# Kernel tuning notes

Measured on AMD Instinct MI355X. Metric: run time of the kernel, lower is better.

Reference implementation:

```python
import jax, jax.numpy as jnp
import numpy as np

S = 64            # rendered_size
CLASS_NUM = 14    # dataset.enc_len
NEG_SLOPE = 0.01
EPS = 1e-5


def _conv(x, w, stride, pad):
    return jax.lax.conv_general_dilated(
        x, w, (stride, stride), [(pad, pad), (pad, pad)],
        dimension_numbers=("NCHW", "OIHW", "NCHW"))


def _bn(x, gamma, beta):
    # BatchNorm2d in training mode: biased batch stats over (N,H,W)
    m = jnp.mean(x, axis=(0, 2, 3), keepdims=True)
    v = jnp.var(x, axis=(0, 2, 3), keepdims=True)
    xn = (x - m) * jax.lax.rsqrt(v + EPS)
    return xn * gamma.reshape(1, -1, 1, 1) + beta.reshape(1, -1, 1, 1)


def _lrelu(x):
    return jnp.where(x >= 0, x, NEG_SLOPE * x)


def _render(elements):
    # elements: (B, N, class_num+4)
    rects = elements[:, :, -4:]
    cls = elements[:, :, :-4]                       # (B, N, C)
    x = rects[:, :, 0][:, :, None, None] * S        # (B, N, 1, 1)
    y = rects[:, :, 1][:, :, None, None] * S
    w = rects[:, :, 2][:, :, None, None] * S
    h = rects[:, :, 3][:, :, None, None] * S
    x0, x1 = x - 0.5 * w, x + 0.5 * w
    y0, y1 = y - 0.5 * h, y + 0.5 * h
    cx = jnp.arange(S, dtype=elements.dtype)[None, None, None, :]  # varies along W
    cy = jnp.arange(S, dtype=elements.dtype)[None, None, :, None]  # varies along H
    k = lambda c, cr: jnp.maximum(1.0 - jnp.abs(c - cr), 0.0)
    b0 = lambda c, cr: jnp.clip(c - cr, 0.0, 1.0)
    b1 = lambda cr, c: jnp.clip(cr - c, 0.0, 1.0)
    by = b0(cy, y0) * b1(y1, cy)                    # (B, N, S, S)
    bx = b0(cx, x0) * b1(x1, cx)
    l0 = k(cx, x0) * by
    l1 = k(cx, x1) * by
    l2 = k(cy, y0) * bx
    l3 = k(cy, y1) * bx
    rendered = jnp.maximum(jnp.maximum(l0, l1), jnp.maximum(l2, l3))  # (B,N,S,S)
    # sum over elements of class one-hot * rendered -> (B, C, S, S)
    return jnp.einsum("bnc,bnhw->bchw", cls, rendered)


def setup_inputs() -> dict:
    key = jax.random.key(0)
    ks = jax.random.split(key, 8)
    B, N = 64, 46
    inp = {
        "input_data": jax.random.uniform(ks[0], (B, N, CLASS_NUM + 4), dtype=jnp.float32),
        "input_length": jax.random.randint(ks[1], (B,), 0, N, dtype=jnp.int32),
        # cnn convs (bias=False) + BN affine params
        "w1": jax.random.normal(ks[2], (64, CLASS_NUM, 5, 5), jnp.float32) * 0.05,
        "g1": jnp.ones((64,), jnp.float32), "b1": jnp.zeros((64,), jnp.float32),
        "w2": jax.random.normal(ks[3], (128, 64, 5, 5), jnp.float32) * 0.03,
        "g2": jnp.ones((128,), jnp.float32), "b2": jnp.zeros((128,), jnp.float32),
        "w3": jax.random.normal(ks[4], (256, 128, 5, 5), jnp.float32) * 0.02,
        "g3": jnp.ones((256,), jnp.float32), "b3": jnp.zeros((256,), jnp.float32),
        # classifier: conv k=8 (bias=False) + BN + 1x1 conv (bias=True)
        "w4": jax.random.normal(ks[5], (1024, 256, 8, 8), jnp.float32) * 0.01,
        "g4": jnp.ones((1024,), jnp.float32), "b4": jnp.zeros((1024,), jnp.float32),
        "w5": jax.random.normal(ks[6], (1, 1024, 1, 1), jnp.float32) * 0.03,
        "b5": jnp.zeros((1,), jnp.float32),
    }
    return inp


def reference(input_data, input_length, w1, g1, b1, w2, g2, b2,
              w3, g3, b3, w4, g4, b4, w5, b5):
    rendered = _render(input_data)                       # (B, C, 64, 64)
    h = _lrelu(_bn(_conv(rendered, w1, 2, 2), g1, b1))   # (B, 64, 32, 32)
    h = _lrelu(_bn(_conv(h, w2, 2, 2), g2, b2))          # (B, 128, 16, 16)
    h = _lrelu(_bn(_conv(h, w3, 2, 2), g3, b3))          # (B, 256, 8, 8)
    h = _lrelu(_bn(_conv(h, w4, 1, 0), g4, b4))          # (B, 1024, 1, 1)
    out = _conv(h, w5, 1, 0) + b5.reshape(1, -1, 1, 1)   # (B, 1, 1, 1)
    return out.squeeze()                                 # (B,)
```

## Files before the change

### kernel.cpp

```cpp
#include <hip/hip_runtime.h>
#include <hip/hip_bf16.h>

#define NEG 0.01f
#define EPS 1e-5f

typedef __attribute__((ext_vector_type(8))) short short8;
typedef __attribute__((ext_vector_type(4))) float floatx4;

__device__ inline unsigned short f2bf(float f) {
    __hip_bfloat16 h = __float2bfloat16(f);
    union { __hip_bfloat16 h; unsigned short u; } cv; cv.h = h;
    return cv.u;
}

__global__ __launch_bounds__(256) void render_kernel(const float* __restrict__ in,
                                                     unsigned short* __restrict__ out) {
    int b = blockIdx.x >> 4;
    int chunk = blockIdx.x & 15;
    __shared__ float r0[46], r1[46], r2[46], r3[46];
    __shared__ float cls_s[46 * 14];
    int tid = threadIdx.x;
    if (tid < 46) {
        const float* p = in + ((size_t)b * 46 + tid) * 18 + 14;
        float x = p[0] * 64.f, y = p[1] * 64.f, w = p[2] * 64.f, h = p[3] * 64.f;
        r0[tid] = x - 0.5f * w; r1[tid] = x + 0.5f * w;
        r2[tid] = y - 0.5f * h; r3[tid] = y + 0.5f * h;
    }
    for (int idx = tid; idx < 46 * 14; idx += 256) {
        int n = idx / 14, c = idx % 14;
        cls_s[idx] = in[((size_t)b * 46 + n) * 18 + c];
    }
    __syncthreads();
    if (tid < 33) {
        int j = chunk * 33 + tid;
        if (j < 528) {
            int y, x;
            if (j < 136) { y = j / 68; x = j - y * 68; }
            else if (j < 272) { int t = j - 136; int yy = t / 68; y = 66 + yy; x = t - yy * 68; }
            else { int t = j - 272; y = 2 + (t >> 2); int k = t & 3; x = (k < 2) ? k : 64 + k; }
            size_t zb = (((size_t)b * 68 + y) * 68 + x) * 16;
            short8 z;
#pragma unroll
            for (int i = 0; i < 8; ++i) z[i] = 0;
            *(short8*)(out + zb) = z;
            *(short8*)(out + zb + 8) = z;
        }
    }
    int pix = chunk * 256 + tid;
    float cx = (float)(pix & 63);
    float cy = (float)(pix >> 6);
    float acc[14];
#pragma unroll
    for (int c = 0; c < 14; ++c) acc[c] = 0.f;
    for (int n = 0; n < 46; ++n) {
        float x0 = r0[n], x1 = r1[n], y0 = r2[n], y1 = r3[n];
        float by = fminf(fmaxf(cy - y0, 0.f), 1.f) * fminf(fmaxf(y1 - cy, 0.f), 1.f);
        float bx = fminf(fmaxf(cx - x0, 0.f), 1.f) * fminf(fmaxf(x1 - cx, 0.f), 1.f);
        float kx0 = fmaxf(1.f - fabsf(cx - x0), 0.f);
        float kx1 = fmaxf(1.f - fabsf(cx - x1), 0.f);
        float ky0 = fmaxf(1.f - fabsf(cy - y0), 0.f);
        float ky1 = fmaxf(1.f - fabsf(cy - y1), 0.f);
        float r = fmaxf(fmaxf(kx0 * by, kx1 * by), fmaxf(ky0 * bx, ky1 * bx));
        if (r > 0.f) {
#pragma unroll
            for (int c = 0; c < 14; ++c) acc[c] = fmaf(cls_s[n * 14 + c], r, acc[c]);
        }
    }
    size_t obase = (((size_t)b * 68 + ((pix >> 6) + 2)) * 68 + ((pix & 63) + 2)) * 16;
    short8 v0, v1;
#pragma unroll
    for (int i = 0; i < 8; ++i) v0[i] = (short)f2bf(acc[i]);
#pragma unroll
    for (int i = 0; i < 6; ++i) v1[i] = (short)f2bf(acc[8 + i]);
    v1[6] = 0; v1[7] = 0;
    *(short8*)(out + obase) = v0;
    *(short8*)(out + obase + 8) = v1;
}

__global__ __launch_bounds__(256) void wtrans_all(const float* __restrict__ w1,
                                                  const float* __restrict__ w2,
                                                  const float* __restrict__ w3,
                                                  unsigned short* __restrict__ wT1,
                                                  unsigned short* __restrict__ wT2,
                                                  unsigned short* __restrict__ wT3) {
    int idx = blockIdx.x * 256 + threadIdx.x;
    const float* w; unsigned short* wT; int CIN, CPLOG, SUB, COLOG;
    if (idx < 30720) { w = w1; wT = wT1; CIN = 14; CPLOG = 4; SUB = 3; COLOG = 6; }
    else if (idx < 235520) { idx -= 30720; w = w2; wT = wT2; CIN = 64; CPLOG = 6; SUB = 10; COLOG = 7; }
    else if (idx < 1054720) { idx -= 235520; w = w3; wT = wT3; CIN = 128; CPLOG = 7; SUB = 20; COLOG = 8; }
    else return;
    int kk = idx & 31;
    int co = (idx >> 5) & ((1 << COLOG) - 1);
    int s = idx >> (5 + COLOG);
    int kh = s / SUB, sub = s - kh * SUB;
    int kidx = sub * 32 + kk;
    int kw = kidx >> CPLOG;
    int ci = kidx & ((1 << CPLOG) - 1);
    float v = (kw < 5 && ci < CIN) ? w[((size_t)(co * CIN + ci) * 5 + kh) * 5 + kw] : 0.f;
    wT[idx] = f2bf(v);
}

template <int CP, int COUT, int HP, int LOG_OHW, int LOG_OW, int SUB,
          int NCO, int NT, int CH, int NW>
__global__ __launch_bounds__(NW * 64) void conv_mfma(
        const unsigned short* __restrict__ inP,
        const unsigned short* __restrict__ wT,
        float* __restrict__ outX,
        float* __restrict__ stacc) {
    constexpr int NSTEP = 5 * SUB;
    constexpr int NCHUNK = NSTEP / CH;
    constexpr int COT = NT * 16;
    constexpr int NSTG = (CH * COT * 4) / (NW * 64);
    static_assert(NSTEP % CH == 0, "CH must divide NSTEP");
    static_assert((CH * COT * 4) % (NW * 64) == 0, "staging must tile evenly");
    __shared__ short Bs[2][CH][COT][32];
    __shared__ float sred[NW][2][COT];
    int tid = threadIdx.x;
    int wave = tid >> 6, lane = tid & 63, q = lane >> 4, l16 = lane & 15;
    int bm = blockIdx.x / NCO, bco = blockIdx.x % NCO;

    const short* aB[4];
#pragma unroll
    for (int f = 0; f < 4; ++f) {
        int m = bm * (NW * 64) + wave * 64 + f * 16 + l16;
        int b = m >> LOG_OHW;
        int ohw = m & ((1 << LOG_OHW) - 1);
        int oh = ohw >> LOG_OW, ow = ohw & ((1 << LOG_OW) - 1);
        aB[f] = (const short*)inP + ((size_t)((b * HP + 2 * oh) * HP + 2 * ow)) * CP + q * 8;
    }
    const short* bgbase = (const short*)wT + (size_t)bco * COT * 32;

    floatx4 acc[4][NT];
#pragma unroll
    for (int f = 0; f < 4; ++f)
#pragma unroll
        for (int nt = 0; nt < NT; ++nt) acc[f][nt] = (floatx4){0.f, 0.f, 0.f, 0.f};

    short8 nb[NSTG];
#pragma unroll
    for (int i = 0; i < NSTG; ++i) {
        int v = tid + i * NW * 64;
        int s = v / (COT * 4);
        int rem = v - s * (COT * 4);
        nb[i] = *(const short8*)(bgbase + ((size_t)s * COUT) * 32 + rem * 8);
    }
#pragma unroll
    for (int i = 0; i < NSTG; ++i) {
        int v = tid + i * NW * 64;
        int s = v / (COT * 4);
        int rem = v - s * (COT * 4);
        *(short8*)((short*)&Bs[0][s][0][0] + rem * 8) = nb[i];
    }
    __syncthreads();

    for (int chunk = 0; chunk < NCHUNK; ++chunk) {
        int cur = chunk & 1;
        if (chunk + 1 < NCHUNK) {
            int step0 = (chunk + 1) * CH;
#pragma unroll
            for (int i = 0; i < NSTG; ++i) {
                int v = tid + i * NW * 64;
                int s = v / (COT * 4);
                int rem = v - s * (COT * 4);
                nb[i] = *(const short8*)(bgbase + ((size_t)(step0 + s) * COUT) * 32 + rem * 8);
            }
        }
#pragma unroll
        for (int s = 0; s < CH; ++s) {
            int step = chunk * CH + s;
            int kh = step / SUB, sub = step - kh * SUB;
            short8 af[4];
#pragma unroll
            for (int f = 0; f < 4; ++f)
                af[f] = *(const short8*)(aB[f] + (size_t)(kh * HP) * CP + sub * 32);
#pragma unroll
            for (int nt = 0; nt < NT; ++nt) {
                short8 bf = *(const short8*)&Bs[cur][s][nt * 16 + l16][q * 8];
#pragma unroll
                for (int f = 0; f < 4; ++f)
                    acc[f][nt] = __builtin_amdgcn_mfma_f32_16x16x32_bf16(af[f], bf, acc[f][nt], 0, 0, 0);
            }
        }
        if (chunk + 1 < NCHUNK) {
#pragma unroll
            for (int i = 0; i < NSTG; ++i) {
                int v = tid + i * NW * 64;
                int s = v / (COT * 4);
                int rem = v - s * (COT * 4);
                *(short8*)((short*)&Bs[cur ^ 1][s][0][0] + rem * 8) = nb[i];
            }
            __syncthreads();
        }
    }
#pragma unroll
    for (int f = 0; f < 4; ++f)
#pragma unroll
        for (int nt = 0; nt < NT; ++nt)
#pragma unroll
            for (int rg = 0; rg < 4; ++rg) {
                int mg = bm * (NW * 64) + wave * 64 + f * 16 + q * 4 + rg;
                int co = bco * COT + nt * 16 + l16;
                outX[(size_t)mg * COUT + co] = acc[f][nt][rg];
            }
#pragma unroll
    for (int nt = 0; nt < NT; ++nt) {
        float s = 0.f, s2 = 0.f;
#pragma unroll
        for (int f = 0; f < 4; ++f)
#pragma unroll
            for (int rg = 0; rg < 4; ++rg) {
                float v = acc[f][nt][rg];
                s += v; s2 = fmaf(v, v, s2);
            }
        s += __shfl_xor(s, 16); s += __shfl_xor(s, 32);
        s2 += __shfl_xor(s2, 16); s2 += __shfl_xor(s2, 32);
        if (q == 0) {
            sred[wave][0][nt * 16 + l16] = s;
            sred[wave][1][nt * 16 + l16] = s2;
        }
    }
    __syncthreads();
    if (tid < COT) {
        float ts = 0.f, ts2 = 0.f;
#pragma unroll
        for (int w = 0; w < NW; ++w) { ts += sred[w][0][tid]; ts2 += sred[w][1][tid]; }
        atomicAdd(&stacc[bco * COT + tid], ts);
        atomicAdd(&stacc[COUT + bco * COT + tid], ts2);
    }
}

__global__ __launch_bounds__(256) void conv4_mfma(const unsigned short* __restrict__ A,
                                                  const float* __restrict__ w4,
                                                  float* __restrict__ h4) {
    constexpr int CH = 4, NCHUNK = 8;
    __shared__ short Bs[CH][64][40];
    int tid = threadIdx.x;
    int bco = blockIdx.x & 15;
    int ks = blockIdx.x >> 4;
    int wave = tid >> 6, lane = tid & 63, q = lane >> 4, l16 = lane & 15;
    const short* aBase = (const short*)A + (size_t)(wave * 16 + l16) * 16384 + ks * 1024 + q * 8;
    int r = tid >> 2, cc = tid & 3;
    const float* bg = w4 + (size_t)(bco * 64 + r) * 16384 + ks * 1024 + cc * 8;

    floatx4 acc[4];
#pragma unroll
    for (int nt = 0; nt < 4; ++nt) acc[nt] = (floatx4){0.f, 0.f, 0.f, 0.f};

    short8 nb[CH];
#pragma unroll
    for (int s = 0; s < CH; ++s) {
        float4 b0 = *(const float4*)(bg + s * 32);
        float4 b1 = *(const float4*)(bg + s * 32 + 4);
        nb[s][0] = (short)f2bf(b0.x); nb[s][1] = (short)f2bf(b0.y);
        nb[s][2] = (short)f2bf(b0.z); nb[s][3] = (short)f2bf(b0.w);
        nb[s][4] = (short)f2bf(b1.x); nb[s][5] = (short)f2bf(b1.y);
        nb[s][6] = (short)f2bf(b1.z); nb[s][7] = (short)f2bf(b1.w);
    }
#pragma unroll
    for (int s = 0; s < CH; ++s) *(short8*)&Bs[s][r][cc * 8] = nb[s];
    __syncthreads();

    for (int chunk = 0; chunk < NCHUNK; ++chunk) {
        bool has_next = (chunk + 1 < NCHUNK);
        if (has_next) {
#pragma unroll
            for (int s = 0; s < CH; ++s) {
                int step = (chunk + 1) * CH + s;
                float4 b0 = *(const float4*)(bg + step * 32);
                float4 b1 = *(const float4*)(bg + step * 32 + 4);
                nb[s][0] = (short)f2bf(b0.x); nb[s][1] = (short)f2bf(b0.y);
                nb[s][2] = (short)f2bf(b0.z); nb[s][3] = (short)f2bf(b0.w);
                nb[s][4] = (short)f2bf(b1.x); nb[s][5] = (short)f2bf(b1.y);
                nb[s][6] = (short)f2bf(b1.z); nb[s][7] = (short)f2bf(b1.w);
            }
        }
#pragma unroll
        for (int s = 0; s < CH; ++s) {
            int step = chunk * CH + s;
            short8 af = *(const short8*)(aBase + step * 32);
#pragma unroll
            for (int nt = 0; nt < 4; ++nt) {
                short8 bf = *(const short8*)&Bs[s][nt * 16 + l16][q * 8];
                acc[nt] = __builtin_amdgcn_mfma_f32_16x16x32_bf16(af, bf, acc[nt], 0, 0, 0);
            }
        }
        if (has_next) {
            __syncthreads();
#pragma unroll
            for (int s = 0; s < CH; ++s) *(short8*)&Bs[s][r][cc * 8] = nb[s];
            __syncthreads();
        }
    }
#pragma unroll
    for (int nt = 0; nt < 4; ++nt) {
#pragma unroll
        for (int rg = 0; rg < 4; ++rg) {
            int mg = wave * 16 + q * 4 + rg;
            int co = bco * 64 + nt * 16 + l16;
            atomicAdd(&h4[(size_t)mg * 1024 + co], acc[nt][rg]);
        }
    }
}

__global__ __launch_bounds__(256) void stats_part(const float* __restrict__ X,
                                                  float* __restrict__ acc,
                                                  int CO, int R, int RPB, int CGLOG) {
    int tid = threadIdx.x;
    int cg = blockIdx.x & ((1 << CGLOG) - 1);
    int rb = blockIdx.x >> CGLOG;
    int c = (cg << 6) + (tid & 63);
    int w = tid >> 6;
    float s = 0.f, s2 = 0.f;
    int rend = min(R, (rb + 1) * RPB);
    for (int r = rb * RPB + w; r < rend; r += 4) {
        float v = X[(size_t)r * CO + c];
        s += v; s2 += v * v;
    }
    __shared__ float ls[4][64], ls2[4][64];
    ls[w][tid & 63] = s; ls2[w][tid & 63] = s2;
    __syncthreads();
    if (tid < 64) {
        float ts = ls[0][tid] + ls[1][tid] + ls[2][tid] + ls[3][tid];
        float ts2 = ls2[0][tid] + ls2[1][tid] + ls2[2][tid] + ls2[3][tid];
        int cc = (cg << 6) + tid;
        atomicAdd(&acc[cc], ts);
        atomicAdd(&acc[CO + cc], ts2);
    }
}

__global__ __launch_bounds__(256) void bnpad_kernel(const float* __restrict__ X,
                                                    const float* __restrict__ stacc,
                                                    const float* __restrict__ g,
                                                    const float* __restrict__ bb,
                                                    unsigned short* __restrict__ out,
                                                    int CO_LOG, int OH, int OHP,
                                                    float invN, int total) {
    int idx = blockIdx.x * 256 + threadIdx.x;
    if (idx >= total) return;
    int CO = 1 << CO_LOG;
    int c = idx & (CO - 1);
    float mean = stacc[c] * invN;
    float var = fmaxf(stacc[CO + c] * invN - mean * mean, 0.f);
    float sc = g[c] * rsqrtf(var + EPS);
    float sh = bb[c] - mean * sc;
    int t = idx >> CO_LOG;
    int x = t % OHP; t /= OHP;
    int y = t % OHP; int b = t / OHP;
    unsigned short v = 0;
    if (y >= 2 && y < OH + 2 && x >= 2 && x < OH + 2) {
        float f = X[(((size_t)(b * OH + (y - 2)) * OH + (x - 2)) << CO_LOG) + c];
        f = f * sc + sh;
        f = f >= 0.f ? f : NEG * f;
        v = f2bf(f);
    }
    out[idx] = v;
}

__global__ __launch_bounds__(256) void bn_nchw_kernel(const float* __restrict__ X,
                                                      const float* __restrict__ stacc,
                                                      const float* __restrict__ g,
                                                      const float* __restrict__ bb,
                                                      unsigned short* __restrict__ out,
                                                      int total) {
    int idx = blockIdx.x * 256 + threadIdx.x;
    if (idx >= total) return;
    int hw = idx & 63;
    int ci = (idx >> 6) & 255;
    int b = idx >> 14;
    float mean = stacc[ci] * (1.f / 4096.f);
    float var = fmaxf(stacc[256 + ci] * (1.f / 4096.f) - mean * mean, 0.f);
    float sc = g[ci] * rsqrtf(var + EPS);
    float sh = bb[ci] - mean * sc;
    float f = X[((size_t)(b * 64 + hw)) * 256 + ci] * sc + sh;
    f = f >= 0.f ? f : NEG * f;
    out[idx] = f2bf(f);
}

__global__ __launch_bounds__(256) void conv5_kernel(const float* __restrict__ X,
                                                    const float* __restrict__ stacc,
                                                    const float* __restrict__ g,
                                                    const float* __restrict__ bb,
                                                    const float* __restrict__ w5,
                                                    const float* __restrict__ b5,
                                                    float* __restrict__ out) {
    int b = blockIdx.x, tid = threadIdx.x;
    float s = 0.f;
    for (int c = tid; c < 1024; c += 256) {
        float mean = stacc[c] * (1.f / 64.f);
        float var = fmaxf(stacc[1024 + c] * (1.f / 64.f) - mean * mean, 0.f);
        float sc = g[c] * rsqrtf(var + EPS);
        float sh = bb[c] - mean * sc;
        float f = X[(size_t)b * 1024 + c] * sc + sh;
        f = f >= 0.f ? f : NEG * f;
        s = fmaf(f, w5[c], s);
    }
#pragma unroll
    for (int off = 32; off > 0; off >>= 1) s += __shfl_down(s, off);
    __shared__ float ls[4];
    if ((tid & 63) == 0) ls[tid >> 6] = s;
    __syncthreads();
    if (tid == 0) out[b] = ls[0] + ls[1] + ls[2] + ls[3] + b5[0];
}

extern "C" void kernel_launch(void* const* d_in, const int* in_sizes, int n_in,
                              void* d_out, int out_size, void* d_ws, size_t ws_size,
                              hipStream_t stream) {
    (void)in_sizes; (void)n_in; (void)out_size; (void)ws_size;
    const float* input_data = (const float*)d_in[0];
    const float* w1 = (const float*)d_in[2];
    const float* g1 = (const float*)d_in[3];
    const float* b1 = (const float*)d_in[4];
    const float* w2 = (const float*)d_in[5];
    const float* g2 = (const float*)d_in[6];
    const float* b2 = (const float*)d_in[7];
    const float* w3 = (const float*)d_in[8];
    const float* g3 = (const float*)d_in[9];
    const float* b3 = (const float*)d_in[10];
    const float* w4 = (const float*)d_in[11];
    const float* g4 = (const float*)d_in[12];
    const float* b4 = (const float*)d_in[13];
    const float* w5 = (const float*)d_in[14];
    const float* b5 = (const float*)d_in[15];

    char* ws = (char*)d_ws;
    float* regA = (float*)ws;
    char* wsB = ws + 16777216;
    char* wsC = wsB + 10616832;
    char* wsD = wsC + 9469952;
    float* h4  = (float*)wsD;
    float* st1 = (float*)(wsD + 262144);
    float* st2 = (float*)(wsD + 262656);
    float* st3 = (float*)(wsD + 263680);
    float* st4 = (float*)(wsD + 265728);
    unsigned short* wT1 = (unsigned short*)(wsD + 274432);
    unsigned short* wT2 = (unsigned short*)(wsD + 335872);
    unsigned short* wT3 = (unsigned short*)(wsD + 745472);

    unsigned short* rendered = (unsigned short*)wsC;
    float* conv1out = regA;
    unsigned short* pad1 = (unsigned short*)wsB;
    float* conv2out = (float*)wsC;
    unsigned short* pad2 = (unsigned short*)wsB;
    float* conv3out = regA;
    unsigned short* a4 = (unsigned short*)wsC;

    hipMemsetAsync(wsD, 0, 273920, stream);
    wtrans_all<<<4120, 256, 0, stream>>>(w1, w2, w3, wT1, wT2, wT3);
    render_kernel<<<1024, 256, 0, stream>>>(input_data, rendered);

    conv_mfma<16, 64, 68, 10, 5, 3, 1, 4, 5, 4><<<256, 256, 0, stream>>>(rendered, wT1, conv1out, st1);
    bnpad_kernel<<<20736, 256, 0, stream>>>(conv1out, st1, g1, b1, pad1, 6, 32, 36, 1.f / 65536.f, 5308416);

    conv_mfma<64, 128, 36, 8, 4, 10, 4, 2, 10, 4><<<256, 256, 0, stream>>>(pad1, wT2, conv2out, st2);
    bnpad_kernel<<<12800, 256, 0, stream>>>(conv2out, st2, g2, b2, pad2, 7, 16, 20, 1.f / 16384.f, 3276800);

    conv_mfma<128, 256, 20, 6, 3, 20, 8, 2, 10, 2><<<256, 128, 0, stream>>>(pad2, wT3, conv3out, st3);
    bn_nchw_kernel<<<4096, 256, 0, stream>>>(conv3out, st3, g3, b3, a4, 1048576);

    conv4_mfma<<<256, 256, 0, stream>>>(a4, w4, h4);
    stats_part<<<16, 256, 0, stream>>>(h4, st4, 1024, 64, 64, 4);

    conv5_kernel<<<64, 256, 0, stream>>>(h4, st4, g4, b4, w5, b5, (float*)d_out);
}
```

Measured before the change: 280.5 us.

## Merge setup kernels, pad LDS weight tiles, halve conv block sizes, fold BN4 stats

Merges the weight-transpose and render kernels into one launch. Pads the shared-memory B tile rows from 32 to 40 shorts to avoid bank conflicts. Retunes the three conv launches to use half the waves per block, twice the blocks and smaller chunks, and doubles the conv4 chunk size. Removes the separate stats kernel by having every conv5 block recompute the per-channel BN statistics itself, which trades a launch for redundant reads of h4.

```diff
diff --git a/kernel.cpp b/kernel.cpp
--- a/kernel.cpp
+++ b/kernel.cpp
@@ -13,12 +13,36 @@
     return cv.u;
 }
 
-__global__ __launch_bounds__(256) void render_kernel(const float* __restrict__ in,
-                                                     unsigned short* __restrict__ out) {
+__global__ __launch_bounds__(256) void head_kernel(const float* __restrict__ in,
+                                                   unsigned short* __restrict__ out,
+                                                   const float* __restrict__ w1,
+                                                   const float* __restrict__ w2,
+                                                   const float* __restrict__ w3,
+                                                   unsigned short* __restrict__ wT1,
+                                                   unsigned short* __restrict__ wT2,
+                                                   unsigned short* __restrict__ wT3) {
+    __shared__ float r0[46], r1[46], r2[46], r3[46];
+    __shared__ float cls_s[46 * 14];
+    if (blockIdx.x >= 1024) {
+        int idx = (blockIdx.x - 1024) * 256 + threadIdx.x;
+        const float* w; unsigned short* wT; int CIN, CPLOG, SUB, COLOG;
+        if (idx < 30720) { w = w1; wT = wT1; CIN = 14; CPLOG = 4; SUB = 3; COLOG = 6; }
+        else if (idx < 235520) { idx -= 30720; w = w2; wT = wT2; CIN = 64; CPLOG = 6; SUB = 10; COLOG = 7; }
+        else if (idx < 1054720) { idx -= 235520; w = w3; wT = wT3; CIN = 128; CPLOG = 7; SUB = 20; COLOG = 8; }
+        else return;
+        int kk = idx & 31;
+        int co = (idx >> 5) & ((1 << COLOG) - 1);
+        int s = idx >> (5 + COLOG);
+        int kh = s / SUB, sub = s - kh * SUB;
+        int kidx = sub * 32 + kk;
+        int kw = kidx >> CPLOG;
+        int ci = kidx & ((1 << CPLOG) - 1);
+        float v = (kw < 5 && ci < CIN) ? w[((size_t)(co * CIN + ci) * 5 + kh) * 5 + kw] : 0.f;
+        wT[idx] = f2bf(v);
+        return;
+    }
     int b = blockIdx.x >> 4;
     int chunk = blockIdx.x & 15;
-    __shared__ float r0[46], r1[46], r2[46], r3[46];
-    __shared__ float cls_s[46 * 14];
     int tid = threadIdx.x;
     if (tid < 46) {
         const float* p = in + ((size_t)b * 46 + tid) * 18 + 14;
@@ -75,29 +99,6 @@
     v1[6] = 0; v1[7] = 0;
     *(short8*)(out + obase) = v0;
     *(short8*)(out + obase + 8) = v1;
-}
-
-__global__ __launch_bounds__(256) void wtrans_all(const float* __restrict__ w1,
-                                                  const float* __restrict__ w2,
-                                                  const float* __restrict__ w3,
-                                                  unsigned short* __restrict__ wT1,
-                                                  unsigned short* __restrict__ wT2,
-                                                  unsigned short* __restrict__ wT3) {
-    int idx = blockIdx.x * 256 + threadIdx.x;
-    const float* w; unsigned short* wT; int CIN, CPLOG, SUB, COLOG;
-    if (idx < 30720) { w = w1; wT = wT1; CIN = 14; CPLOG = 4; SUB = 3; COLOG = 6; }
-    else if (idx < 235520) { idx -= 30720; w = w2; wT = wT2; CIN = 64; CPLOG = 6; SUB = 10; COLOG = 7; }
-    else if (idx < 1054720) { idx -= 235520; w = w3; wT = wT3; CIN = 128; CPLOG = 7; SUB = 20; COLOG = 8; }
-    else return;
-    int kk = idx & 31;
-    int co = (idx >> 5) & ((1 << COLOG) - 1);
-    int s = idx >> (5 + COLOG);
-    int kh = s / SUB, sub = s - kh * SUB;
-    int kidx = sub * 32 + kk;
-    int kw = kidx >> CPLOG;
-    int ci = kidx & ((1 << CPLOG) - 1);
-    float v = (kw < 5 && ci < CIN) ? w[((size_t)(co * CIN + ci) * 5 + kh) * 5 + kw] : 0.f;
-    wT[idx] = f2bf(v);
 }
 
 template <int CP, int COUT, int HP, int LOG_OHW, int LOG_OW, int SUB,
@@ -113,7 +114,7 @@
     constexpr int NSTG = (CH * COT * 4) / (NW * 64);
     static_assert(NSTEP % CH == 0, "CH must divide NSTEP");
     static_assert((CH * COT * 4) % (NW * 64) == 0, "staging must tile evenly");
-    __shared__ short Bs[2][CH][COT][32];
+    __shared__ short __attribute__((aligned(16))) Bs[2][CH][COT][40];
     __shared__ float sred[NW][2][COT];
     int tid = threadIdx.x;
     int wave = tid >> 6, lane = tid & 63, q = lane >> 4, l16 = lane & 15;
@@ -149,7 +150,7 @@
         int v = tid + i * NW * 64;
         int s = v / (COT * 4);
         int rem = v - s * (COT * 4);
-        *(short8*)((short*)&Bs[0][s][0][0] + rem * 8) = nb[i];
+        *(short8*)&Bs[0][s][rem >> 2][(rem & 3) * 8] = nb[i];
     }
     __syncthreads();
 
@@ -187,7 +188,7 @@
                 int v = tid + i * NW * 64;
                 int s = v / (COT * 4);
                 int rem = v - s * (COT * 4);
-                *(short8*)((short*)&Bs[cur ^ 1][s][0][0] + rem * 8) = nb[i];
+                *(short8*)&Bs[cur ^ 1][s][rem >> 2][(rem & 3) * 8] = nb[i];
             }
             __syncthreads();
         }
@@ -232,8 +233,8 @@
 __global__ __launch_bounds__(256) void conv4_mfma(const unsigned short* __restrict__ A,
                                                   const float* __restrict__ w4,
                                                   float* __restrict__ h4) {
-    constexpr int CH = 4, NCHUNK = 8;
-    __shared__ short Bs[CH][64][40];
+    constexpr int CH = 8, NCHUNK = 4;
+    __shared__ short __attribute__((aligned(16))) Bs[CH][64][40];
     int tid = threadIdx.x;
     int bco = blockIdx.x & 15;
     int ks = blockIdx.x >> 4;
@@ -299,32 +300,6 @@
             int co = bco * 64 + nt * 16 + l16;
             atomicAdd(&h4[(size_t)mg * 1024 + co], acc[nt][rg]);
         }
-    }
-}
-
-__global__ __launch_bounds__(256) void stats_part(const float* __restrict__ X,
-                                                  float* __restrict__ acc,
-                                                  int CO, int R, int RPB, int CGLOG) {
-    int tid = threadIdx.x;
-    int cg = blockIdx.x & ((1 << CGLOG) - 1);
-    int rb = blockIdx.x >> CGLOG;
-    int c = (cg << 6) + (tid & 63);
-    int w = tid >> 6;
-    float s = 0.f, s2 = 0.f;
-    int rend = min(R, (rb + 1) * RPB);
-    for (int r = rb * RPB + w; r < rend; r += 4) {
-        float v = X[(size_t)r * CO + c];
-        s += v; s2 += v * v;
-    }
-    __shared__ float ls[4][64], ls2[4][64];
-    ls[w][tid & 63] = s; ls2[w][tid & 63] = s2;
-    __syncthreads();
-    if (tid < 64) {
-        float ts = ls[0][tid] + ls[1][tid] + ls[2][tid] + ls[3][tid];
-        float ts2 = ls2[0][tid] + ls2[1][tid] + ls2[2][tid] + ls2[3][tid];
-        int cc = (cg << 6) + tid;
-        atomicAdd(&acc[cc], ts);
-        atomicAdd(&acc[CO + cc], ts2);
     }
 }
 
@@ -376,21 +351,31 @@
     out[idx] = f2bf(f);
 }
 
-__global__ __launch_bounds__(256) void conv5_kernel(const float* __restrict__ X,
-                                                    const float* __restrict__ stacc,
+__global__ __launch_bounds__(256) void conv5_kernel(const float* __restrict__ h4,
                                                     const float* __restrict__ g,
                                                     const float* __restrict__ bb,
                                                     const float* __restrict__ w5,
                                                     const float* __restrict__ b5,
                                                     float* __restrict__ out) {
+    __shared__ float scs[1024], shs[1024];
     int b = blockIdx.x, tid = threadIdx.x;
+    for (int c = tid; c < 1024; c += 256) {
+        float s = 0.f, s2 = 0.f;
+#pragma unroll 4
+        for (int r = 0; r < 64; ++r) {
+            float v = h4[(size_t)r * 1024 + c];
+            s += v; s2 = fmaf(v, v, s2);
+        }
+        float mean = s * (1.f / 64.f);
+        float var = fmaxf(s2 * (1.f / 64.f) - mean * mean, 0.f);
+        float sc = g[c] * rsqrtf(var + EPS);
+        scs[c] = sc;
+        shs[c] = bb[c] - mean * sc;
+    }
+    __syncthreads();
     float s = 0.f;
     for (int c = tid; c < 1024; c += 256) {
-        float mean = stacc[c] * (1.f / 64.f);
-        float var = fmaxf(stacc[1024 + c] * (1.f / 64.f) - mean * mean, 0.f);
-        float sc = g[c] * rsqrtf(var + EPS);
-        float sh = bb[c] - mean * sc;
-        float f = X[(size_t)b * 1024 + c] * sc + sh;
+        float f = h4[(size_t)b * 1024 + c] * scs[c] + shs[c];
         f = f >= 0.f ? f : NEG * f;
         s = fmaf(f, w5[c], s);
     }
@@ -431,7 +416,6 @@
     float* st1 = (float*)(wsD + 262144);
     float* st2 = (float*)(wsD + 262656);
     float* st3 = (float*)(wsD + 263680);
-    float* st4 = (float*)(wsD + 265728);
     unsigned short* wT1 = (unsigned short*)(wsD + 274432);
     unsigned short* wT2 = (unsigned short*)(wsD + 335872);
     unsigned short* wT3 = (unsigned short*)(wsD + 745472);
@@ -445,20 +429,18 @@
     unsigned short* a4 = (unsigned short*)wsC;
 
     hipMemsetAsync(wsD, 0, 273920, stream);
-    wtrans_all<<<4120, 256, 0, stream>>>(w1, w2, w3, wT1, wT2, wT3);
-    render_kernel<<<1024, 256, 0, stream>>>(input_data, rendered);
-
-    conv_mfma<16, 64, 68, 10, 5, 3, 1, 4, 5, 4><<<256, 256, 0, stream>>>(rendered, wT1, conv1out, st1);
+    head_kernel<<<5144, 256, 0, stream>>>(input_data, rendered, w1, w2, w3, wT1, wT2, wT3);
+
+    conv_mfma<16, 64, 68, 10, 5, 3, 1, 4, 3, 2><<<512, 128, 0, stream>>>(rendered, wT1, conv1out, st1);
     bnpad_kernel<<<20736, 256, 0, stream>>>(conv1out, st1, g1, b1, pad1, 6, 32, 36, 1.f / 65536.f, 5308416);
 
-    conv_mfma<64, 128, 36, 8, 4, 10, 4, 2, 10, 4><<<256, 256, 0, stream>>>(pad1, wT2, conv2out, st2);
+    conv_mfma<64, 128, 36, 8, 4, 10, 4, 2, 5, 2><<<512, 128, 0, stream>>>(pad1, wT2, conv2out, st2);
     bnpad_kernel<<<12800, 256, 0, stream>>>(conv2out, st2, g2, b2, pad2, 7, 16, 20, 1.f / 16384.f, 3276800);
 
-    conv_mfma<128, 256, 20, 6, 3, 20, 8, 2, 10, 2><<<256, 128, 0, stream>>>(pad2, wT3, conv3out, st3);
+    conv_mfma<128, 256, 20, 6, 3, 20, 8, 2, 5, 1><<<512, 64, 0, stream>>>(pad2, wT3, conv3out, st3);
     bn_nchw_kernel<<<4096, 256, 0, stream>>>(conv3out, st3, g3, b3, a4, 1048576);
 
     conv4_mfma<<<256, 256, 0, stream>>>(a4, w4, h4);
-    stats_part<<<16, 256, 0, stream>>>(h4, st4, 1024, 64, 64, 4);
-
-    conv5_kernel<<<64, 256, 0, stream>>>(h4, st4, g4, b4, w5, b5, (float*)d_out);
-}
+
+    conv5_kernel<<<64, 256, 0, stream>>>(h4, g4, b4, w5, b5, (float*)d_out);
+}
```

Measured after the change: 308.1 us. 1.1x slower.
